# Kernel tuning notes

Hardware: AMD Instinct MI355X
Metric: run time of the kernel (lower is better)

## Reference

```python
import jax, jax.numpy as jnp
import numpy as np

B, N, INPUT_DIM, SELF_DIM = 8192, 96, 64, 16
HUMAN_DIM = INPUT_DIM - SELF_DIM  # 48


def setup_inputs() -> dict:
    key = jax.random.key(0)
    ks = jax.random.split(key, 8)
    inp = {
        "state": jax.random.normal(ks[0], (B, N, INPUT_DIM), dtype=jnp.float32),
        # t MLP: Linear(16,50) -> ReLU -> Linear(50,48)
        "t_w1": jax.random.normal(ks[1], (SELF_DIM, 50), dtype=jnp.float32) * 0.1,
        "t_b1": jnp.zeros((50,), dtype=jnp.float32),
        "t_w2": jax.random.normal(ks[2], (50, HUMAN_DIM), dtype=jnp.float32) * 0.1,
        "t_b2": jnp.zeros((HUMAN_DIM,), dtype=jnp.float32),
        # attention weight (scaled to keep softmax unsaturated)
        "w_a": jax.random.normal(ks[3], (HUMAN_DIM, HUMAN_DIM), dtype=jnp.float32) * 0.02,
        # graph-conv weights
        "w1": jax.random.normal(ks[4], (HUMAN_DIM, 64), dtype=jnp.float32) * 0.1,
        "w2": jax.random.normal(ks[5], (64, 64), dtype=jnp.float32) * 0.1,
        # value head: Linear(64,64) -> ReLU -> Linear(64,1)
        "v_w1": jax.random.normal(ks[6], (64, 64), dtype=jnp.float32) * 0.1,
        "v_b1": jnp.zeros((64,), dtype=jnp.float32),
        "v_w2": jax.random.normal(ks[7], (64, 1), dtype=jnp.float32) * 0.1,
        "v_b2": jnp.zeros((1,), dtype=jnp.float32),
    }
    return inp


def reference(state, t_w1, t_b1, t_w2, t_b2, w_a, w1, w2, v_w1, v_b1, v_w2, v_b2):
    # self-state MLP (t_mlp=True path), extra ReLU applied on MLP output
    self_state = state[:, 0, :SELF_DIM]                       # [B, S]
    human = state[:, :, SELF_DIM:]                            # [B, N, H]
    h = jax.nn.relu(self_state @ t_w1 + t_b1)                 # [B, 50]
    new_self = jax.nn.relu(h @ t_w2 + t_b2)[:, None, :]       # [B, 1, H]
    X = jnp.concatenate([new_self, human], axis=1)            # [B, N+1, H]
    # attention-weighted adjacency: softmax(X W_a X^T) over last dim
    scores = jnp.einsum('bnh,hk,bmk->bnm', X, w_a, X)         # [B, N+1, N+1]
    A = jax.nn.softmax(scores, axis=2)
    # two graph-conv layers (num_layer == 2, expand_x=False)
    h1 = jax.nn.relu(jnp.einsum('bnm,bmh,hk->bnk', A, X, w1))   # [B, N+1, 64]
    h2 = jax.nn.relu(jnp.einsum('bnm,bmh,hk->bnk', A, h1, w2))  # [B, N+1, 64]
    feat = h2[:, 0, :]                                        # [B, 64]
    # value head MLP (planning_mlp=True)
    value = jax.nn.relu(feat @ v_w1 + v_b1) @ v_w2 + v_b2     # [B, 1]
    return value
```

## Files before the change

### kernel.cpp

```cpp
#include <hip/hip_runtime.h>


#define XP (97 * 16)
#define ES 104
#define WS 56

typedef short bf16x8 __attribute__((ext_vector_type(8)));
typedef float f32x4 __attribute__((ext_vector_type(4)));

__device__ __forceinline__ unsigned rtne_hi(float f) {
    unsigned u = __float_as_uint(f);
    return (u + 0x7fffu + ((u >> 16) & 1u)) & 0xffff0000u;
}
__device__ __forceinline__ void split2(float f, unsigned short* h, unsigned short* l) {
    unsigned hb = rtne_hi(f);
    float r = f - __uint_as_float(hb);
    *h = (unsigned short)(hb >> 16);
    *l = (unsigned short)(__float_as_uint(r) >> 16);
}
__device__ __forceinline__ unsigned short rtne16(float f) {
    return (unsigned short)(rtne_hi(f) >> 16);
}
__device__ __forceinline__ float bf2f(unsigned short u) {
    return __uint_as_float(((unsigned)u) << 16);
}
__device__ __forceinline__ bf16x8 ldf(const unsigned short* p) {
    return *(const bf16x8*)p;
}

__global__ void vnet_prep(const float* __restrict__ w_a, const float* __restrict__ w1,
                          unsigned short* __restrict__ ws) {
    unsigned short* waT_h = ws;
    unsigned short* waT_l = ws + 2304;
    unsigned short* w1T_h = ws + 4608;
    unsigned short* w1T_l = ws + 4608 + 3072;
    for (int i = threadIdx.x; i < 48 * 48; i += blockDim.x) {
        int c = i / 48, k = i % 48;
        unsigned short h, l; split2(w_a[k * 48 + c], &h, &l);
        waT_h[i] = h; waT_l[i] = l;
    }
    for (int i = threadIdx.x; i < 64 * 48; i += blockDim.x) {
        int lo = i / 48, j = i % 48;
        unsigned short h, l; split2(w1[j * 64 + lo], &h, &l);
        w1T_h[i] = h; w1T_l[i] = l;
    }
}

__global__ __launch_bounds__(256, 4)
void vnet_kernel(const float* __restrict__ state,
                 const float* __restrict__ t_w1, const float* __restrict__ t_b1,
                 const float* __restrict__ t_w2, const float* __restrict__ t_b2,
                 const float* __restrict__ w2,   const float* __restrict__ v_w1,
                 const float* __restrict__ v_b1, const float* __restrict__ v_w2,
                 const float* __restrict__ v_b2, const unsigned short* __restrict__ ws,
                 float* __restrict__ out)
{
    __shared__ __align__(16) unsigned short Xh[3 * XP], Xl[3 * XP];
    __shared__ __align__(16) unsigned short Eh[16 * ES];
    __shared__ __align__(16) unsigned short W0h[16 * WS], W0l[16 * WS];
    __shared__ __align__(16) unsigned short W1h[16 * WS], W1l[16 * WS];
    __shared__ float a0c[112];
    __shared__ float invb[16];
    __shared__ float e96[16];
    __shared__ float pacc[64];
    __shared__ float psum[64];

    const unsigned short* waT_h = ws;
    const unsigned short* waT_l = ws + 2304;
    const unsigned short* w1T_h = ws + 4608;
    const unsigned short* w1T_l = ws + 4608 + 3072;

    const int tid  = threadIdx.x;
    const int w    = tid >> 6;
    const int lane = tid & 63;
    const int row  = lane & 15;
    const int quad = lane >> 4;
    const int b    = blockIdx.x;
    const float* sb = state + (size_t)b * (96 * 64);
    const bf16x8 ZF = {0, 0, 0, 0, 0, 0, 0, 0};

    if (tid < 16) pacc[tid] = sb[tid];
    for (int i = tid; i < 96 * 12; i += 256) {
        int r = i / 12, q = i % 12;
        float4 v = *(const float4*)(sb + r * 64 + 16 + 4 * q);
        unsigned short h0, l0, h1v, l1, h2, l2, h3, l3;
        split2(v.x, &h0, &l0); split2(v.y, &h1v, &l1);
        split2(v.z, &h2, &l2); split2(v.w, &h3, &l3);
        int m = 1 + r;
        int o = (q >> 2) * XP + m * 16 + (q & 3) * 4;
        *(uint2*)&Xh[o] = make_uint2((unsigned)h0 | ((unsigned)h1v << 16),
                                     (unsigned)h2 | ((unsigned)h3 << 16));
        *(uint2*)&Xl[o] = make_uint2((unsigned)l0 | ((unsigned)l1 << 16),
                                     (unsigned)l2 | ((unsigned)l3 << 16));
    }
    __syncthreads();

    if (tid < 50) {
        float a = t_b1[tid];
        #pragma unroll
        for (int i = 0; i < 16; ++i) a = fmaf(pacc[i], t_w1[i * 50 + tid], a);
        a0c[tid] = fmaxf(a, 0.f);
    }
    __syncthreads();
    if (tid < 48) {
        float a = t_b2[tid];
        for (int i = 0; i < 50; ++i) a = fmaf(a0c[i], t_w2[i * 48 + tid], a);
        unsigned short h, l; split2(fmaxf(a, 0.f), &h, &l);
        int o = (tid >> 4) * XP + (tid & 15);
        Xh[o] = h; Xl[o] = l;
    }
    if (tid >= 64 && tid < 128) pacc[tid - 64] = 0.f;
    if (tid >= 128 && tid < 143) a0c[tid - 31] = 0.f;
    __syncthreads();

    bf16x8 B4h[3], B4l[3];
    if (w < 3) {
        #pragma unroll
        for (int c3 = 0; c3 < 3; ++c3) {
            bf16x8 th, tl;
            #pragma unroll
            for (int j = 0; j < 8; ++j) {
                int e = w * XP + (32 * c3 + 8 * quad + j) * 16 + row;
                th[j] = (short)Xh[e];
                tl[j] = (short)Xl[e];
            }
            B4h[c3] = th;
            B4l[c3] = tl;
        }
    } else {
        #pragma unroll
        for (int c3 = 0; c3 < 3; ++c3) { B4h[c3] = ZF; B4l[c3] = ZF; }
    }

    {
        if (w < 3) {
            f32x4 acc = {0.f, 0.f, 0.f, 0.f};
            #pragma unroll
            for (int ch = 0; ch < 2; ++ch) {
                int kb = 16 * ch;
                int c = kb + quad * 8;
                int o = (c >> 4) * XP + row * 16 + (c & 15);
                bf16x8 ah = ldf(&Xh[o]);
                bf16x8 al = ldf(&Xl[o]);
                if (ch == 1 && quad < 2) { ah = ZF; al = ZF; }
                bf16x8 bh = ldf(waT_h + (16 * w + row) * 48 + kb + quad * 8);
                bf16x8 bl = ldf(waT_l + (16 * w + row) * 48 + kb + quad * 8);
                acc = __builtin_amdgcn_mfma_f32_16x16x32_bf16(ah, bh, acc, 0, 0, 0);
                acc = __builtin_amdgcn_mfma_f32_16x16x32_bf16(ah, bl, acc, 0, 0, 0);
                acc = __builtin_amdgcn_mfma_f32_16x16x32_bf16(al, bh, acc, 0, 0, 0);
            }
            #pragma unroll
            for (int r = 0; r < 4; ++r) {
                unsigned short h, l; split2(acc[r], &h, &l);
                W0h[(quad * 4 + r) * WS + 16 * w + row] = h;
                W0l[(quad * 4 + r) * WS + 16 * w + row] = l;
            }
        }
    }
    __syncthreads();
    {
        bf16x8 a0h = ldf(&W0h[row * WS + quad * 8]);
        bf16x8 a0l = ldf(&W0l[row * WS + quad * 8]);
        bf16x8 a1h = ldf(&W0h[row * WS + 16 + quad * 8]);
        bf16x8 a1l = ldf(&W0l[row * WS + 16 + quad * 8]);
        if (quad < 2) { a1h = ZF; a1l = ZF; }
        float ps0 = 0.f, ps1 = 0.f, ps2 = 0.f, ps3 = 0.f;
        for (int t = w; t < 6; t += 4) {
            int m = 16 * t + row;
            f32x4 acc = {0.f, 0.f, 0.f, 0.f};
            int o0 = (quad >> 1) * XP + m * 16 + (quad & 1) * 8;
            bf16x8 bh = ldf(&Xh[o0]);
            bf16x8 bl = ldf(&Xl[o0]);
            acc = __builtin_amdgcn_mfma_f32_16x16x32_bf16(a0h, bh, acc, 0, 0, 0);
            acc = __builtin_amdgcn_mfma_f32_16x16x32_bf16(a0h, bl, acc, 0, 0, 0);
            acc = __builtin_amdgcn_mfma_f32_16x16x32_bf16(a0l, bh, acc, 0, 0, 0);
            bh = ldf(&Xh[o0 + XP]);
            bl = ldf(&Xl[o0 + XP]);
            acc = __builtin_amdgcn_mfma_f32_16x16x32_bf16(a1h, bh, acc, 0, 0, 0);
            acc = __builtin_amdgcn_mfma_f32_16x16x32_bf16(a1h, bl, acc, 0, 0, 0);
            acc = __builtin_amdgcn_mfma_f32_16x16x32_bf16(a1l, bh, acc, 0, 0, 0);
            float e0v = __expf(acc[0]), e1v = __expf(acc[1]);
            float e2v = __expf(acc[2]), e3v = __expf(acc[3]);
            Eh[(quad * 4 + 0) * ES + m] = rtne16(e0v);
            Eh[(quad * 4 + 1) * ES + m] = rtne16(e1v);
            Eh[(quad * 4 + 2) * ES + m] = rtne16(e2v);
            Eh[(quad * 4 + 3) * ES + m] = rtne16(e3v);
            if (quad == 0) a0c[m] = e0v;
            ps0 += e0v; ps1 += e1v; ps2 += e2v; ps3 += e3v;
        }
        #pragma unroll
        for (int d = 1; d < 16; d <<= 1) {
            ps0 += __shfl_xor(ps0, d); ps1 += __shfl_xor(ps1, d);
            ps2 += __shfl_xor(ps2, d); ps3 += __shfl_xor(ps3, d);
        }
        if (row == 0) {
            psum[w * 16 + quad * 4 + 0] = ps0;
            psum[w * 16 + quad * 4 + 1] = ps1;
            psum[w * 16 + quad * 4 + 2] = ps2;
            psum[w * 16 + quad * 4 + 3] = ps3;
        }
    }
    __syncthreads();

    for (int s = 0; s < 7; ++s) {
        unsigned short* Wsh = (s & 1) ? W1h : W0h;
        unsigned short* Wsl = (s & 1) ? W1l : W0l;
        unsigned short* Wnh = (s & 1) ? W0h : W1h;
        unsigned short* Wnl = (s & 1) ? W0l : W1l;

        if (s < 6 && w < 3) {
            f32x4 acc = {0.f, 0.f, 0.f, 0.f};
            int n = (s + 1) * 16 + row; int nc = n < 97 ? n : 96;
            #pragma unroll
            for (int ch = 0; ch < 2; ++ch) {
                int kb = 16 * ch;
                int c = kb + quad * 8;
                int o = (c >> 4) * XP + nc * 16 + (c & 15);
                bf16x8 ah = ldf(&Xh[o]);
                bf16x8 al = ldf(&Xl[o]);
                if (ch == 1 && quad < 2) { ah = ZF; al = ZF; }
                bf16x8 bh = ldf(waT_h + (16 * w + row) * 48 + kb + quad * 8);
                bf16x8 bl = ldf(waT_l + (16 * w + row) * 48 + kb + quad * 8);
                acc = __builtin_amdgcn_mfma_f32_16x16x32_bf16(ah, bh, acc, 0, 0, 0);
                acc = __builtin_amdgcn_mfma_f32_16x16x32_bf16(ah, bl, acc, 0, 0, 0);
                acc = __builtin_amdgcn_mfma_f32_16x16x32_bf16(al, bh, acc, 0, 0, 0);
            }
            #pragma unroll
            for (int r = 0; r < 4; ++r) {
                unsigned short h, l; split2(acc[r], &h, &l);
                Wnh[(quad * 4 + r) * WS + 16 * w + row] = h;
                Wnl[(quad * 4 + r) * WS + 16 * w + row] = l;
            }
        }
        {
            int rw = tid >> 4, mg = tid & 15;
            float s96 = 0.f;
            #pragma unroll
            for (int kk = 0; kk < 3; ++kk) {
                int c = mg + 16 * kk;
                float xw = bf2f(Wsh[rw * WS + c]) + bf2f(Wsl[rw * WS + c]);
                float xv = bf2f(Xh[kk * XP + 1536 + mg]) + bf2f(Xl[kk * XP + 1536 + mg]);
                s96 = fmaf(xw, xv, s96);
            }
            s96 += __shfl_xor(s96, 1); s96 += __shfl_xor(s96, 2);
            s96 += __shfl_xor(s96, 4); s96 += __shfl_xor(s96, 8);
            float e0 = __expf(s96);
            float sum = (mg < 4) ? psum[mg * 16 + rw] : 0.f;
            if (mg == 0) sum += e0;
            sum += __shfl_xor(sum, 1); sum += __shfl_xor(sum, 2);
            sum += __shfl_xor(sum, 4); sum += __shfl_xor(sum, 8);
            if (mg == 0) {
                e96[rw] = e0;
                invb[rw] = 1.f / sum;
                if (s == 0 && rw == 0) a0c[96] = e0;
            }
        }
        __syncthreads();

        if (w < 3) {
            f32x4 acc = {0.f, 0.f, 0.f, 0.f};
            #pragma unroll
            for (int c3 = 0; c3 < 3; ++c3) {
                int mb = 32 * c3;
                bf16x8 ah = ldf(&Eh[row * ES + mb + quad * 8]);
                acc = __builtin_amdgcn_mfma_f32_16x16x32_bf16(ah, B4h[c3], acc, 0, 0, 0);
                acc = __builtin_amdgcn_mfma_f32_16x16x32_bf16(ah, B4l[c3], acc, 0, 0, 0);
            }
            int j = 16 * w + row;
            float xv = bf2f(Xh[w * XP + 1536 + row]) + bf2f(Xl[w * XP + 1536 + row]);
            #pragma unroll
            for (int r = 0; r < 4; ++r) {
                float v = fmaf(e96[quad * 4 + r], xv, acc[r]) * invb[quad * 4 + r];
                unsigned short h, l; split2(v, &h, &l);
                Wsh[(quad * 4 + r) * WS + j] = h;
                Wsl[(quad * 4 + r) * WS + j] = l;
            }
        } else if (s == 0) {
            float iv0 = invb[0];
            for (int m = lane; m < 97; m += 64) a0c[m] *= iv0;
        }
        __syncthreads();

        {
            f32x4 acc = {0.f, 0.f, 0.f, 0.f};
            #pragma unroll
            for (int ch = 0; ch < 2; ++ch) {
                int kb = 16 * ch;
                bf16x8 ah = ldf(&Wsh[row * WS + kb + quad * 8]);
                bf16x8 al = ldf(&Wsl[row * WS + kb + quad * 8]);
                if (ch == 1 && quad < 2) { ah = ZF; al = ZF; }
                bf16x8 bh = ldf(w1T_h + (16 * w + row) * 48 + kb + quad * 8);
                bf16x8 bl = ldf(w1T_l + (16 * w + row) * 48 + kb + quad * 8);
                acc = __builtin_amdgcn_mfma_f32_16x16x32_bf16(ah, bh, acc, 0, 0, 0);
                acc = __builtin_amdgcn_mfma_f32_16x16x32_bf16(ah, bl, acc, 0, 0, 0);
                acc = __builtin_amdgcn_mfma_f32_16x16x32_bf16(al, bh, acc, 0, 0, 0);
            }
            float part = 0.f;
            #pragma unroll
            for (int r = 0; r < 4; ++r)
                part += fmaxf(acc[r], 0.f) * a0c[s * 16 + quad * 4 + r];
            part += __shfl_xor(part, 16);
            part += __shfl_xor(part, 32);
            if (quad == 0) pacc[16 * w + row] += part;
        }
        if (s < 6) {
            bf16x8 a0h = ldf(&Wnh[row * WS + quad * 8]);
            bf16x8 a0l = ldf(&Wnl[row * WS + quad * 8]);
            bf16x8 a1h = ldf(&Wnh[row * WS + 16 + quad * 8]);
            bf16x8 a1l = ldf(&Wnl[row * WS + 16 + quad * 8]);
            if (quad < 2) { a1h = ZF; a1l = ZF; }
            float ps0 = 0.f, ps1 = 0.f, ps2 = 0.f, ps3 = 0.f;
            for (int t = w; t < 6; t += 4) {
                int m = 16 * t + row;
                f32x4 acc = {0.f, 0.f, 0.f, 0.f};
                int o0 = (quad >> 1) * XP + m * 16 + (quad & 1) * 8;
                bf16x8 bh = ldf(&Xh[o0]);
                bf16x8 bl = ldf(&Xl[o0]);
                acc = __builtin_amdgcn_mfma_f32_16x16x32_bf16(a0h, bh, acc, 0, 0, 0);
                acc = __builtin_amdgcn_mfma_f32_16x16x32_bf16(a0h, bl, acc, 0, 0, 0);
                acc = __builtin_amdgcn_mfma_f32_16x16x32_bf16(a0l, bh, acc, 0, 0, 0);
                bh = ldf(&Xh[o0 + XP]);
                bl = ldf(&Xl[o0 + XP]);
                acc = __builtin_amdgcn_mfma_f32_16x16x32_bf16(a1h, bh, acc, 0, 0, 0);
                acc = __builtin_amdgcn_mfma_f32_16x16x32_bf16(a1h, bl, acc, 0, 0, 0);
                acc = __builtin_amdgcn_mfma_f32_16x16x32_bf16(a1l, bh, acc, 0, 0, 0);
                float e0v = __expf(acc[0]), e1v = __expf(acc[1]);
                float e2v = __expf(acc[2]), e3v = __expf(acc[3]);
                Eh[(quad * 4 + 0) * ES + m] = rtne16(e0v);
                Eh[(quad * 4 + 1) * ES + m] = rtne16(e1v);
                Eh[(quad * 4 + 2) * ES + m] = rtne16(e2v);
                Eh[(quad * 4 + 3) * ES + m] = rtne16(e3v);
                ps0 += e0v; ps1 += e1v; ps2 += e2v; ps3 += e3v;
            }
            #pragma unroll
            for (int d = 1; d < 16; d <<= 1) {
                ps0 += __shfl_xor(ps0, d); ps1 += __shfl_xor(ps1, d);
                ps2 += __shfl_xor(ps2, d); ps3 += __shfl_xor(ps3, d);
            }
            if (row == 0) {
                psum[w * 16 + quad * 4 + 0] = ps0;
                psum[w * 16 + quad * 4 + 1] = ps1;
                psum[w * 16 + quad * 4 + 2] = ps2;
                psum[w * 16 + quad * 4 + 3] = ps3;
            }
        }
        __syncthreads();
    }

    float* featb = a0c;
    if (tid < 64) {
        float a = 0.f;
        #pragma unroll 8
        for (int l = 0; l < 64; ++l) a = fmaf(pacc[l], w2[l * 64 + tid], a);
        featb[tid] = fmaxf(a, 0.f);
    }
    __syncthreads();
    if (tid < 64) {
        float a = v_b1[tid];
        #pragma unroll 8
        for (int c = 0; c < 64; ++c) a = fmaf(featb[c], v_w1[c * 64 + tid], a);
        float qd = fmaxf(a, 0.f) * v_w2[tid];
        #pragma unroll
        for (int d = 32; d >= 1; d >>= 1) qd += __shfl_xor(qd, d);
        if (tid == 0) out[b] = qd + v_b2[0];
    }
}

extern "C" void kernel_launch(void* const* d_in, const int* in_sizes, int n_in,
                              void* d_out, int out_size, void* d_ws, size_t ws_size,
                              hipStream_t stream) {
    (void)n_in; (void)ws_size; (void)out_size;
    const float* state = (const float*)d_in[0];
    const float* t_w1  = (const float*)d_in[1];
    const float* t_b1  = (const float*)d_in[2];
    const float* t_w2  = (const float*)d_in[3];
    const float* t_b2  = (const float*)d_in[4];
    const float* w_a   = (const float*)d_in[5];
    const float* w1    = (const float*)d_in[6];
    const float* w2    = (const float*)d_in[7];
    const float* v_w1  = (const float*)d_in[8];
    const float* v_b1  = (const float*)d_in[9];
    const float* v_w2  = (const float*)d_in[10];
    const float* v_b2  = (const float*)d_in[11];
    unsigned short* ws = (unsigned short*)d_ws;
    const int nb = in_sizes[0] / (96 * 64);

    vnet_prep<<<1, 256, 0, stream>>>(w_a, w1, ws);
    vnet_kernel<<<nb, 256, 0, stream>>>(state, t_w1, t_b1, t_w2, t_b2, w2,
                                        v_w1, v_b1, v_w2, v_b2, ws, (float*)d_out);
}
```

Baseline: 468.1 us.

## Defer softmax normalization and remove one barrier per attention stage

Result: faster. 453.9 us (-3.0%).

```diff
diff --git a/kernel.cpp b/kernel.cpp
--- a/kernel.cpp
+++ b/kernel.cpp
@@ -60,10 +60,11 @@
     __shared__ __align__(16) unsigned short W0h[16 * WS], W0l[16 * WS];
     __shared__ __align__(16) unsigned short W1h[16 * WS], W1l[16 * WS];
     __shared__ float a0c[112];
-    __shared__ float invb[16];
-    __shared__ float e96[16];
+    __shared__ float e96b[2][16];
+    __shared__ float psum[2][64];
+    __shared__ float invbS[16];
     __shared__ float pacc[64];
-    __shared__ float psum[64];
+    __shared__ float inv0s;
 
     const unsigned short* waT_h = ws;
     const unsigned short* waT_l = ws + 2304;
@@ -194,10 +195,28 @@
             ps2 += __shfl_xor(ps2, d); ps3 += __shfl_xor(ps3, d);
         }
         if (row == 0) {
-            psum[w * 16 + quad * 4 + 0] = ps0;
-            psum[w * 16 + quad * 4 + 1] = ps1;
-            psum[w * 16 + quad * 4 + 2] = ps2;
-            psum[w * 16 + quad * 4 + 3] = ps3;
+            psum[0][w * 16 + quad * 4 + 0] = ps0;
+            psum[0][w * 16 + quad * 4 + 1] = ps1;
+            psum[0][w * 16 + quad * 4 + 2] = ps2;
+            psum[0][w * 16 + quad * 4 + 3] = ps3;
+        }
+        {
+            int rw = tid >> 4, mg = tid & 15;
+            float s96 = 0.f;
+            #pragma unroll
+            for (int kk = 0; kk < 3; ++kk) {
+                int c = mg + 16 * kk;
+                float xw = bf2f(W0h[rw * WS + c]) + bf2f(W0l[rw * WS + c]);
+                float xv = bf2f(Xh[kk * XP + 1536 + mg]) + bf2f(Xl[kk * XP + 1536 + mg]);
+                s96 = fmaf(xw, xv, s96);
+            }
+            s96 += __shfl_xor(s96, 1); s96 += __shfl_xor(s96, 2);
+            s96 += __shfl_xor(s96, 4); s96 += __shfl_xor(s96, 8);
+            if (mg == 0) {
+                float e0 = __expf(s96);
+                e96b[0][rw] = e0;
+                if (rw == 0) a0c[96] = e0;
+            }
         }
     }
     __syncthreads();
@@ -207,77 +226,61 @@
         unsigned short* Wsl = (s & 1) ? W1l : W0l;
         unsigned short* Wnh = (s & 1) ? W0h : W1h;
         unsigned short* Wnl = (s & 1) ? W0l : W1l;
-
-        if (s < 6 && w < 3) {
-            f32x4 acc = {0.f, 0.f, 0.f, 0.f};
-            int n = (s + 1) * 16 + row; int nc = n < 97 ? n : 96;
-            #pragma unroll
-            for (int ch = 0; ch < 2; ++ch) {
-                int kb = 16 * ch;
-                int c = kb + quad * 8;
-                int o = (c >> 4) * XP + nc * 16 + (c & 15);
-                bf16x8 ah = ldf(&Xh[o]);
-                bf16x8 al = ldf(&Xl[o]);
-                if (ch == 1 && quad < 2) { ah = ZF; al = ZF; }
-                bf16x8 bh = ldf(waT_h + (16 * w + row) * 48 + kb + quad * 8);
-                bf16x8 bl = ldf(waT_l + (16 * w + row) * 48 + kb + quad * 8);
-                acc = __builtin_amdgcn_mfma_f32_16x16x32_bf16(ah, bh, acc, 0, 0, 0);
-                acc = __builtin_amdgcn_mfma_f32_16x16x32_bf16(ah, bl, acc, 0, 0, 0);
-                acc = __builtin_amdgcn_mfma_f32_16x16x32_bf16(al, bh, acc, 0, 0, 0);
-            }
-            #pragma unroll
-            for (int r = 0; r < 4; ++r) {
-                unsigned short h, l; split2(acc[r], &h, &l);
-                Wnh[(quad * 4 + r) * WS + 16 * w + row] = h;
-                Wnl[(quad * 4 + r) * WS + 16 * w + row] = l;
-            }
-        }
-        {
-            int rw = tid >> 4, mg = tid & 15;
-            float s96 = 0.f;
-            #pragma unroll
-            for (int kk = 0; kk < 3; ++kk) {
-                int c = mg + 16 * kk;
-                float xw = bf2f(Wsh[rw * WS + c]) + bf2f(Wsl[rw * WS + c]);
-                float xv = bf2f(Xh[kk * XP + 1536 + mg]) + bf2f(Xl[kk * XP + 1536 + mg]);
-                s96 = fmaf(xw, xv, s96);
-            }
-            s96 += __shfl_xor(s96, 1); s96 += __shfl_xor(s96, 2);
-            s96 += __shfl_xor(s96, 4); s96 += __shfl_xor(s96, 8);
-            float e0 = __expf(s96);
-            float sum = (mg < 4) ? psum[mg * 16 + rw] : 0.f;
-            if (mg == 0) sum += e0;
-            sum += __shfl_xor(sum, 1); sum += __shfl_xor(sum, 2);
-            sum += __shfl_xor(sum, 4); sum += __shfl_xor(sum, 8);
-            if (mg == 0) {
-                e96[rw] = e0;
-                invb[rw] = 1.f / sum;
-                if (s == 0 && rw == 0) a0c[96] = e0;
-            }
-        }
-        __syncthreads();
+        const int sb_ = s & 1;
 
         if (w < 3) {
-            f32x4 acc = {0.f, 0.f, 0.f, 0.f};
-            #pragma unroll
-            for (int c3 = 0; c3 < 3; ++c3) {
-                int mb = 32 * c3;
-                bf16x8 ah = ldf(&Eh[row * ES + mb + quad * 8]);
-                acc = __builtin_amdgcn_mfma_f32_16x16x32_bf16(ah, B4h[c3], acc, 0, 0, 0);
-                acc = __builtin_amdgcn_mfma_f32_16x16x32_bf16(ah, B4l[c3], acc, 0, 0, 0);
-            }
-            int j = 16 * w + row;
-            float xv = bf2f(Xh[w * XP + 1536 + row]) + bf2f(Xl[w * XP + 1536 + row]);
-            #pragma unroll
-            for (int r = 0; r < 4; ++r) {
-                float v = fmaf(e96[quad * 4 + r], xv, acc[r]) * invb[quad * 4 + r];
-                unsigned short h, l; split2(v, &h, &l);
-                Wsh[(quad * 4 + r) * WS + j] = h;
-                Wsl[(quad * 4 + r) * WS + j] = l;
-            }
-        } else if (s == 0) {
-            float iv0 = invb[0];
-            for (int m = lane; m < 97; m += 64) a0c[m] *= iv0;
+            {
+                f32x4 acc = {0.f, 0.f, 0.f, 0.f};
+                #pragma unroll
+                for (int c3 = 0; c3 < 3; ++c3) {
+                    int mb = 32 * c3;
+                    bf16x8 ah = ldf(&Eh[row * ES + mb + quad * 8]);
+                    acc = __builtin_amdgcn_mfma_f32_16x16x32_bf16(ah, B4h[c3], acc, 0, 0, 0);
+                    acc = __builtin_amdgcn_mfma_f32_16x16x32_bf16(ah, B4l[c3], acc, 0, 0, 0);
+                }
+                int j = 16 * w + row;
+                float xv = bf2f(Xh[w * XP + 1536 + row]) + bf2f(Xl[w * XP + 1536 + row]);
+                #pragma unroll
+                for (int r = 0; r < 4; ++r) {
+                    float v = fmaf(e96b[sb_][quad * 4 + r], xv, acc[r]);
+                    unsigned short h, l; split2(v, &h, &l);
+                    Wsh[(quad * 4 + r) * WS + j] = h;
+                    Wsl[(quad * 4 + r) * WS + j] = l;
+                }
+            }
+            if (s < 6) {
+                f32x4 acc = {0.f, 0.f, 0.f, 0.f};
+                int n = (s + 1) * 16 + row; int nc = n < 97 ? n : 96;
+                #pragma unroll
+                for (int ch = 0; ch < 2; ++ch) {
+                    int kb = 16 * ch;
+                    int c = kb + quad * 8;
+                    int o = (c >> 4) * XP + nc * 16 + (c & 15);
+                    bf16x8 ah = ldf(&Xh[o]);
+                    bf16x8 al = ldf(&Xl[o]);
+                    if (ch == 1 && quad < 2) { ah = ZF; al = ZF; }
+                    bf16x8 bh = ldf(waT_h + (16 * w + row) * 48 + kb + quad * 8);
+                    bf16x8 bl = ldf(waT_l + (16 * w + row) * 48 + kb + quad * 8);
+                    acc = __builtin_amdgcn_mfma_f32_16x16x32_bf16(ah, bh, acc, 0, 0, 0);
+                    acc = __builtin_amdgcn_mfma_f32_16x16x32_bf16(ah, bl, acc, 0, 0, 0);
+                    acc = __builtin_amdgcn_mfma_f32_16x16x32_bf16(al, bh, acc, 0, 0, 0);
+                }
+                #pragma unroll
+                for (int r = 0; r < 4; ++r) {
+                    unsigned short h, l; split2(acc[r], &h, &l);
+                    Wnh[(quad * 4 + r) * WS + 16 * w + row] = h;
+                    Wnl[(quad * 4 + r) * WS + 16 * w + row] = l;
+                }
+            }
+        } else {
+            if (lane < 16) {
+                float sden = psum[sb_][lane] + psum[sb_][16 + lane]
+                           + psum[sb_][32 + lane] + psum[sb_][48 + lane]
+                           + e96b[sb_][lane];
+                float iv = 1.f / sden;
+                invbS[lane] = iv;
+                if (s == 0 && lane == 0) inv0s = iv;
+            }
         }
         __syncthreads();
 
@@ -297,8 +300,10 @@
             }
             float part = 0.f;
             #pragma unroll
-            for (int r = 0; r < 4; ++r)
-                part += fmaxf(acc[r], 0.f) * a0c[s * 16 + quad * 4 + r];
+            for (int r = 0; r < 4; ++r) {
+                int n = quad * 4 + r;
+                part += fmaxf(acc[r], 0.f) * (a0c[s * 16 + n] * invbS[n]);
+            }
             part += __shfl_xor(part, 16);
             part += __shfl_xor(part, 32);
             if (quad == 0) pacc[16 * w + row] += part;
@@ -337,11 +342,26 @@
                 ps0 += __shfl_xor(ps0, d); ps1 += __shfl_xor(ps1, d);
                 ps2 += __shfl_xor(ps2, d); ps3 += __shfl_xor(ps3, d);
             }
+            const int nb2 = (s + 1) & 1;
             if (row == 0) {
-                psum[w * 16 + quad * 4 + 0] = ps0;
-                psum[w * 16 + quad * 4 + 1] = ps1;
-                psum[w * 16 + quad * 4 + 2] = ps2;
-                psum[w * 16 + quad * 4 + 3] = ps3;
+                psum[nb2][w * 16 + quad * 4 + 0] = ps0;
+                psum[nb2][w * 16 + quad * 4 + 1] = ps1;
+                psum[nb2][w * 16 + quad * 4 + 2] = ps2;
+                psum[nb2][w * 16 + quad * 4 + 3] = ps3;
+            }
+            {
+                int rw = tid >> 4, mg = tid & 15;
+                float s96 = 0.f;
+                #pragma unroll
+                for (int kk = 0; kk < 3; ++kk) {
+                    int c = mg + 16 * kk;
+                    float xw = bf2f(Wnh[rw * WS + c]) + bf2f(Wnl[rw * WS + c]);
+                    float xv = bf2f(Xh[kk * XP + 1536 + mg]) + bf2f(Xl[kk * XP + 1536 + mg]);
+                    s96 = fmaf(xw, xv, s96);
+                }
+                s96 += __shfl_xor(s96, 1); s96 += __shfl_xor(s96, 2);
+                s96 += __shfl_xor(s96, 4); s96 += __shfl_xor(s96, 8);
+                if (mg == 0) e96b[nb2][rw] = __expf(s96);
             }
         }
         __syncthreads();
@@ -352,7 +372,7 @@
         float a = 0.f;
         #pragma unroll 8
         for (int l = 0; l < 64; ++l) a = fmaf(pacc[l], w2[l * 64 + tid], a);
-        featb[tid] = fmaxf(a, 0.f);
+        featb[tid] = fmaxf(a * inv0s, 0.f);
     }
     __syncthreads();
     if (tid < 64) {
```
